# Kernel optimization log

Measured on AMD Instinct MI355X. Metric: run time of the kernel, lower is better.

## Reference

```python
import jax, jax.numpy as jnp
import numpy as np

B, N, H, HEADS, L = 8, 64, 512, 8, 4
VOCAB, NBOND, CLS = 128, 8, 2
SP = H // HEADS
SCALE = float(np.sqrt(H))  # module divides by sqrt(hidden_dim), not sqrt(sp_dim)


def _ln(x):
    # fresh nn.LayerNorm each call -> gamma=1, beta=0
    m = jnp.mean(x, -1, keepdims=True)
    v = jnp.mean((x - m) ** 2, -1, keepdims=True)
    return (x - m) / jnp.sqrt(v + 1e-5)


def _split(x):  # [B,N,H] -> [B,h,N,sp]
    return x.reshape(B, N, HEADS, SP).transpose(0, 2, 1, 3)


def setup_inputs() -> dict:
    key = jax.random.key(0)
    ks = jax.random.split(key, 16)
    s = 0.05
    return {
        "input_batch": jax.random.randint(ks[0], (B, N), 0, VOCAB),
        "adj_m": jax.random.randint(ks[1], (B, N, N), 0, NBOND),
        "atom_emb": jax.random.normal(ks[2], (VOCAB, H), jnp.float32) * s,
        "bond_emb": jax.random.normal(ks[3], (NBOND, H), jnp.float32) * s,
        "Wq": jax.random.normal(ks[4], (L, H, H), jnp.float32) * s,
        "Wk": jax.random.normal(ks[5], (L, H, H), jnp.float32) * s,
        "Wv": jax.random.normal(ks[6], (L, H, H), jnp.float32) * s,
        "Wew": jax.random.normal(ks[7], (L, H, H), jnp.float32) * s,
        "Wstack": jax.random.normal(ks[8], (L, H, H), jnp.float32) * s,
        "Wf1": jax.random.normal(ks[9], (L, H, 4 * H), jnp.float32) * s,
        "Wf2": jax.random.normal(ks[10], (L, 4 * H, H), jnp.float32) * s,
        "Wout": jax.random.normal(ks[11], (H, H), jnp.float32) * s,
        "Wpred": jax.random.normal(ks[12], (H, CLS), jnp.float32) * s,
        "bpred": jnp.zeros((CLS,), jnp.float32),
    }


def _forward(input_batch, adj_m, atom_emb, bond_emb, Wq, Wk, Wv, Wew,
             Wstack, Wf1, Wf2, Wout, Wpred, bpred):
    x = atom_emb[input_batch]        # [B,N,H] atom embeddings
    bond = bond_emb[adj_m]           # [B,N,N,H] bond embeddings
    neg = jnp.where(adj_m > 0, 0.0, -jnp.inf)[:, None, :, :]  # [B,1,N,N]
    for l in range(L):
        xn = _ln(x)
        q = _split(xn @ Wq[l])
        k = _split(xn @ Wk[l])
        v = _split(xn @ Wv[l])
        ew = bond @ Wew[l]           # [B,N,N,H]
        w = ew.reshape(B, N, N, HEADS, SP).transpose(0, 3, 1, 2, 4)  # [B,h,N,N,sp]
        # bond_influence==1: sim_ij = q_i . (k_j + w_ij)
        logits = jnp.einsum('bhid,bhjd->bhij', q, k) \
               + jnp.einsum('bhid,bhijd->bhij', q, w)
        attn = jax.nn.softmax(logits / SCALE + neg, axis=-1)
        o = jnp.einsum('bhij,bhjd->bhid', attn, v)
        o = o.transpose(0, 2, 1, 3).reshape(B, N, H) @ Wstack[l]
        attn_resid = o + xn
        ff = jax.nn.relu(_ln(attn_resid) @ Wf1[l]) @ Wf2[l]
        x = ff + attn_resid          # transformer_output
        # edge attention update: softmax over {w.w, w.x_i, w.x_j}
        ew_s = jnp.sum(ew * ew, -1)                      # [B,N,N]
        a0 = jnp.einsum('bijh,bih->bij', ew, x)
        a1 = jnp.einsum('bijh,bjh->bij', ew, x)
        wgt = jax.nn.softmax(jnp.stack([ew_s, a0, a1], -1) / SCALE, -1)  # [B,N,N,3]
        bond = (wgt[..., 0:1] * ew
                + wgt[..., 1:2] * x[:, :, None, :]
                + wgt[..., 2:3] * x[:, None, :, :])      # new edge state
    cls = jnp.tanh(x[:, 0, :] @ Wout)
    return jax.nn.softmax(cls @ Wpred + bpred, axis=-1)


def reference(input_batch, adj_m, atom_emb, bond_emb, Wq, Wk, Wv, Wew,
              Wstack, Wf1, Wf2, Wout, Wpred, bpred):
    return _forward(input_batch, adj_m, atom_emb, bond_emb, Wq, Wk, Wv, Wew,
                    Wstack, Wf1, Wf2, Wout, Wpred, bpred)
```

## Files before the change

### kernel.cpp

```cpp
#include <hip/hip_runtime.h>
#include <hip/hip_bf16.h>

typedef __hip_bfloat16 bf16;

#define B_     8
#define N_     64
#define H_     512
#define HEADS_ 8
#define SP_    64
#define L_     4
static constexpr float INV_SCALE = 0.044194173824159216f;

typedef __attribute__((ext_vector_type(8))) short short8;
typedef __attribute__((ext_vector_type(4))) float f32x4;

__device__ __forceinline__ void unpack8(uint4 u, float* f) {
    f[0] = __uint_as_float(u.x << 16); f[1] = __uint_as_float(u.x & 0xffff0000u);
    f[2] = __uint_as_float(u.y << 16); f[3] = __uint_as_float(u.y & 0xffff0000u);
    f[4] = __uint_as_float(u.z << 16); f[5] = __uint_as_float(u.z & 0xffff0000u);
    f[6] = __uint_as_float(u.w << 16); f[7] = __uint_as_float(u.w & 0xffff0000u);
}

__device__ __forceinline__ bf16 f2bf(float v) { return __float2bfloat16(v); }

__device__ __forceinline__ uint4 pack8bf(float4 a, float4 b) {
    __align__(16) bf16 t[8];
    t[0] = f2bf(a.x); t[1] = f2bf(a.y); t[2] = f2bf(a.z); t[3] = f2bf(a.w);
    t[4] = f2bf(b.x); t[5] = f2bf(b.y); t[6] = f2bf(b.z); t[7] = f2bf(b.w);
    return *(const uint4*)t;
}

#define RSTR 80

template <int EPI>
__device__ __forceinline__ void gemm64_body(char* lds,
        const bf16* __restrict__ A, const bf16* __restrict__ Bt,
        void* __restrict__ Cv, const float* __restrict__ R,
        int M, int N, int K, int bx, int by, int kbeg, int kend) {
    char* As = lds;
    char* Bs = lds + 2 * 64 * RSTR;
    const int tid = threadIdx.x;
    const int bm = bx * 64, bn = by * 64;
    const int w = tid >> 6, lane = tid & 63;
    const int wr = (w >> 1) * 32, wc = (w & 1) * 32;
    const int m0 = lane & 15, q4 = lane >> 4;

    f32x4 acc[2][2] = {};

    const int rA = tid >> 3;
    const int cA = tid & 7;
    const int ksP = cA >> 2;
    const int cB = (cA & 3) * 16;
    const int cE = cA * 8;

    for (int k0 = kbeg; k0 < kend; k0 += 64) {
        uint4 a0 = *(const uint4*)(A  + (size_t)(bm + rA) * K + k0 + cE);
        uint4 a1 = *(const uint4*)(A  + (size_t)(bm + rA + 32) * K + k0 + cE);
        uint4 b0 = *(const uint4*)(Bt + (size_t)(bn + rA) * K + k0 + cE);
        uint4 b1 = *(const uint4*)(Bt + (size_t)(bn + rA + 32) * K + k0 + cE);
        __syncthreads();
        *(uint4*)(As + ksP * (64 * RSTR) + rA * RSTR + cB) = a0;
        *(uint4*)(As + ksP * (64 * RSTR) + (rA + 32) * RSTR + cB) = a1;
        *(uint4*)(Bs + ksP * (64 * RSTR) + rA * RSTR + cB) = b0;
        *(uint4*)(Bs + ksP * (64 * RSTR) + (rA + 32) * RSTR + cB) = b1;
        __syncthreads();
        short8 af[2][2], bfr[2][2];
        #pragma unroll
        for (int ks = 0; ks < 2; ++ks)
            #pragma unroll
            for (int t = 0; t < 2; ++t) {
                af[ks][t]  = *(const short8*)(As + ks * (64 * RSTR) + (wr + t * 16 + m0) * RSTR + q4 * 16);
                bfr[ks][t] = *(const short8*)(Bs + ks * (64 * RSTR) + (wc + t * 16 + m0) * RSTR + q4 * 16);
            }
        #pragma unroll
        for (int ks = 0; ks < 2; ++ks)
            #pragma unroll
            for (int mt = 0; mt < 2; ++mt)
                #pragma unroll
                for (int nt = 0; nt < 2; ++nt)
                    acc[mt][nt] = __builtin_amdgcn_mfma_f32_16x16x32_bf16(
                        af[ks][mt], bfr[ks][nt], acc[mt][nt], 0, 0, 0);
    }
// ... 4 lines not shown
        for (int mt = 0; mt < 2; ++mt)
            #pragma unroll
            for (int i = 0; i < 4; ++i) {
                int row = bm + wr + mt * 16 + q4 * 4 + i;
                #pragma unroll
                for (int nt = 0; nt < 2; ++nt) {
                    int col = bn + wc + nt * 16 + m0;
                    float v = acc[mt][nt][i];
                    if (EPI == 1) v += R[(size_t)row * N + col];
                    C[(size_t)row * N + col] = v;
                }
            }
    } else {
        bf16* C = (bf16*)Cv;
        #pragma unroll
        for (int mt = 0; mt < 2; ++mt)
            #pragma unroll
            for (int i = 0; i < 4; ++i) {
                int row = bm + wr + mt * 16 + q4 * 4 + i;
                #pragma unroll
                for (int nt = 0; nt < 2; ++nt) {
                    int col = bn + wc + nt * 16 + m0;
                    float v = acc[mt][nt][i];
                    if (EPI == 2) v = fmaxf(v, 0.0f);
                    C[(size_t)row * N + col] = __float2bfloat16(v);
                }
            }
    }
}

template <int EPI, bool SPLIT>
__launch_bounds__(256)
__global__ void mfma_gemm_s(const bf16* __restrict__ A, const bf16* __restrict__ Bt,
                            void* __restrict__ Cv, const float* __restrict__ R,
                            int M, int N, int K) {
    __shared__ __align__(16) char lds[4 * 64 * RSTR];
    int kbeg = 0, kend = K;
    const bf16* B2 = Bt;
    void* C2 = Cv;
    if (SPLIT) {
        int ks = K / gridDim.z;
        kbeg = blockIdx.z * ks;
        kend = kbeg + ks;
        C2 = (void*)((float*)Cv + (size_t)blockIdx.z * M * N);
        gemm64_body<0>(lds, A, B2, C2, nullptr, M, N, K, blockIdx.x, blockIdx.y, kbeg, kend);
    } else {
        B2 = Bt + (size_t)blockIdx.z * N * K;
        if (EPI <= 1) C2 = (void*)((float*)Cv + (size_t)blockIdx.z * M * N);
        gemm64_body<EPI>(lds, A, B2, C2, R, M, N, K, blockIdx.x, blockIdx.y, kbeg, kend);
    }
}


__device__ __forceinline__ void ptable_body(char* lds, const float* __restrict__ q,
        const bf16* __restrict__ Bt, float* __restrict__ P, int b, int h, bool shr) {
    char* As = lds;
    char* Bs = lds + 2 * 64 * RSTR;
    const int tid = threadIdx.x;
    const int w = tid >> 6, lane = tid & 63;
    const int wr = (w >> 1) * 32, wc = (w & 1) * 32;
    const int m0 = lane & 15, q4 = lane >> 4;
    const int rA = tid >> 3;
    const int cA = tid & 7;
    const int ksP = cA >> 2;
    const int cB = (cA & 3) * 16;
    const int cE = cA * 8;

    const float* Aq = q + (size_t)(b * 64) * 512 + h * 64;
    const bf16*  Bb = Bt + (shr ? (size_t)0 : (size_t)b * 64 * 512) + h * 64;

    float4 fa0 = *(const float4*)(Aq + (size_t)rA * 512 + cE);
    float4 fa1 = *(const float4*)(Aq + (size_t)rA * 512 + cE + 4);
    float4 fb0 = *(const float4*)(Aq + (size_t)(rA + 32) * 512 + cE);
    float4 fb1 = *(const float4*)(Aq + (size_t)(rA + 32) * 512 + cE + 4);
    uint4 bv0 = *(const uint4*)(Bb + (size_t)rA * 512 + cE);
    uint4 bv1 = *(const uint4*)(Bb + (size_t)(rA + 32) * 512 + cE);
    uint4 av0 = pack8bf(fa0, fa1);
    uint4 av1 = pack8bf(fb0, fb1);
    *(uint4*)(As + ksP * (64 * RSTR) + rA * RSTR + cB) = av0;
    *(uint4*)(As + ksP * (64 * RSTR) + (rA + 32) * RSTR + cB) = av1;
    *(uint4*)(Bs + ksP * (64 * RSTR) + rA * RSTR + cB) = bv0;
    *(uint4*)(Bs + ksP * (64 * RSTR) + (rA + 32) * RSTR + cB) = bv1;
    __syncthreads();

    f32x4 acc[2][2] = {};
    short8 af[2][2], bfr[2][2];
    #pragma unroll
    for (int ks = 0; ks < 2; ++ks)
        #pragma unroll
        for (int t = 0; t < 2; ++t) {
            af[ks][t]  = *(const short8*)(As + ks * (64 * RSTR) + (wr + t * 16 + m0) * RSTR + q4 * 16);
            bfr[ks][t] = *(const short8*)(Bs + ks * (64 * RSTR) + (wc + t * 16 + m0) * RSTR + q4 * 16);
        }
    #pragma unroll
    for (int ks = 0; ks < 2; ++ks)
        #pragma unroll
        for (int mt = 0; mt < 2; ++mt)
            #pragma unroll
            for (int nt = 0; nt < 2; ++nt)
                acc[mt][nt] = __builtin_amdgcn_mfma_f32_16x16x32_bf16(
                    af[ks][mt], bfr[ks][nt], acc[mt][nt], 0, 0, 0);

    #pragma unroll
    for (int mt = 0; mt < 2; ++mt)
        #pragma unroll
        for (int i = 0; i < 4; ++i) {
            int row = wr + mt * 16 + q4 * 4 + i;
            #pragma unroll
            for (int nt = 0; nt < 2; ++nt) {
                int col = wc + nt * 16 + m0;
                P[(((size_t)b * 8 + h) * 64 + row) * 64 + col] = acc[mt][nt][i];
            }
        }
}

__device__ __forceinline__ void ugemm_body(char* lds, const float* __restrict__ q,
        const bf16* __restrict__ wc3, bf16* __restrict__ ubf, int h, int mb, int nb) {
    char* As = lds;
    char* Bs = lds + 2 * 64 * RSTR;
    const int tid = threadIdx.x;
    const int w = tid >> 6, lane = tid & 63;
    const int wr = (w >> 1) * 32, wc = (w & 1) * 32;
    const int m0 = lane & 15, q4 = lane >> 4;
    const int rA = tid >> 3;
    const int cA = tid & 7;
    const int ksP = cA >> 2;
    const int cB = (cA & 3) * 16;
    const int cE = cA * 8;

    const float* Aq = q + (size_t)(mb * 64) * 512 + h * 64;
    const bf16*  Bt = wc3 + (size_t)(nb * 64) * 512 + h * 64;

    float4 fa0 = *(const float4*)(Aq + (size_t)rA * 512 + cE);
    float4 fa1 = *(const float4*)(Aq + (size_t)rA * 512 + cE + 4);
    float4 fb0 = *(const float4*)(Aq + (size_t)(rA + 32) * 512 + cE);
    float4 fb1 = *(const float4*)(Aq + (size_t)(rA + 32) * 512 + cE + 4);
    uint4 b0 = *(const uint4*)(Bt + (size_t)rA * 512 + cE);
    uint4 b1 = *(const uint4*)(Bt + (size_t)(rA + 32) * 512 + cE);
    uint4 a0 = pack8bf(fa0, fa1);
    uint4 a1 = pack8bf(fb0, fb1);
    *(uint4*)(As + ksP * (64 * RSTR) + rA * RSTR + cB) = a0;
    *(uint4*)(As + ksP * (64 * RSTR) + (rA + 32) * RSTR + cB) = a1;
    *(uint4*)(Bs + ksP * (64 * RSTR) + rA * RSTR + cB) = b0;
    *(uint4*)(Bs + ksP * (64 * RSTR) + (rA + 32) * RSTR + cB) = b1;
    __syncthreads();

    f32x4 acc[2][2] = {};
    short8 af[2][2], bfr[2][2];
    #pragma unroll
    for (int ks = 0; ks < 2; ++ks)
        #pragma unroll
        for (int t = 0; t < 2; ++t) {
            af[ks][t]  = *(const short8*)(As + ks * (64 * RSTR) + (wr + t * 16 + m0) * RSTR + q4 * 16);
            bfr[ks][t] = *(const short8*)(Bs + ks * (64 * RSTR) + (wc + t * 16 + m0) * RSTR + q4 * 16);
        }
    #pragma unroll
    for (int ks = 0; ks < 2; ++ks)
        #pragma unroll
        for (int mt = 0; mt < 2; ++mt)
            #pragma unroll
            for (int nt = 0; nt < 2; ++nt)
                acc[mt][nt] = __builtin_amdgcn_mfma_f32_16x16x32_bf16(
                    af[ks][mt], bfr[ks][nt], acc[mt][nt], 0, 0, 0);

    #pragma unroll
    for (int mt = 0; mt < 2; ++mt)
        #pragma unroll
        for (int i = 0; i < 4; ++i) {
            int row = mb * 64 + wr + mt * 16 + q4 * 4 + i;
            #pragma unroll
            for (int nt = 0; nt < 2; ++nt) {
                int col = nb * 64 + wc + nt * 16 + m0;
                ubf[(size_t)row * 4096 + h * 512 + col] = f2bf(acc[mt][nt][i]);
            }
        }
}

__device__ __forceinline__ void coeff0_body(const int* __restrict__ adj,
        const float* __restrict__ gbuf, int row, int j,
        float* __restrict__ w0o, float* __restrict__ w1o, float* __restrict__ w2o) {
    int b = row >> 6, i = row & 63;
    int p = row * 64 + j;
    int t = adj[p];
    const float* G0  = gbuf + 5 * 32768 + (size_t)b * 4096;
    const float* TEE = gbuf + 6 * 32768;
    float s0 = TEE[t * 64 + t];
    float s1 = G0[t * 64 + i];
    float s2 = G0[t * 64 + j];
    float t0 = s0 * INV_SCALE, t1 = s1 * INV_SCALE, t2 = s2 * INV_SCALE;
    float m = fmaxf(t0, fmaxf(t1, t2));
    float e0 = expf(t0 - m), e1 = expf(t1 - m), e2 = expf(t2 - m);
    float inv = 1.0f / (e0 + e1 + e2);
    w0o[p] = e0 * inv;
    w1o[p] = e1 * inv;
    w2o[p] = e2 * inv;
}

__device__ __forceinline__ void coeff1_body(const int* __restrict__ adj,
        const float* __restrict__ c0a, const float* __restrict__ c1a, const float* __restrict__ c2a,
        const float* __restrict__ gbuf, int row, int j,
        float* __restrict__ w0o, float* __restrict__ w1o, float* __restrict__ w2o) {
    int b = row >> 6, i = row & 63;
    int p = row * 64 + j;
    int t = adj[p];
    const float* TXX = gbuf + 0 * 32768 + (size_t)b * 4096;
    const float* TEX = gbuf + 1 * 32768 + (size_t)b * 4096;
    const float* TXx = gbuf + 2 * 32768 + (size_t)b * 4096;
    const float* TEx = gbuf + 3 * 32768 + (size_t)b * 4096;
    const float* TEE = gbuf + 4 * 32768 + (size_t)b * 4096;
    float c0 = c0a[p], c1 = c1a[p], c2 = c2a[p];
    float s1 = c0 * TEx[t * 64 + i] + c1 * TXx[i * 64 + i] + c2 * TXx[j * 64 + i];
    float s2 = c0 * TEx[t * 64 + j] + c1 * TXx[i * 64 + j] + c2 * TXx[j * 64 + j];
    float s0 = c0 * c0 * TEE[t * 64 + t] + c1 * c1 * TXX[i * 64 + i] + c2 * c2 * TXX[j * 64 + j]
             + 2.f * c0 * c1 * TEX[t * 64 + i] + 2.f * c0 * c2 * TEX[t * 64 + j]
             + 2.f * c1 * c2 * TXX[i * 64 + j];
    float t0 = s0 * INV_SCALE, t1 = s1 * INV_SCALE, t2 = s2 * INV_SCALE;
    float m = fmaxf(t0, fmaxf(t1, t2));
    float e0 = expf(t0 - m), e1 = expf(t1 - m), e2 = expf(t2 - m);
    float inv = 1.0f / (e0 + e1 + e2);
    w0o[p] = e0 * inv;
    w1o[p] = e1 * inv;
    w2o[p] = e2 * inv;
}

__device__ __forceinline__ void coeff2_body(const int* __restrict__ adj,
        const float* __restrict__ c0a, const float* __restrict__ c1a, const float* __restrict__ c2a,
        const float* __restrict__ c0b, const float* __restrict__ c1b, const float* __restrict__ c2b,
        const float* __restrict__ gbuf, int row, int j,
        float* __restrict__ w0o, float* __restrict__ w1o, float* __restrict__ w2o) {
    int b = row >> 6, i = row & 63;
    int p = row * 64 + j;
    int t = adj[p];
    const float* TXX = gbuf + 0 * 32768 + (size_t)b * 4096;
    const float* TXY = gbuf + 1 * 32768 + (size_t)b * 4096;
    const float* TYY = gbuf + 2 * 32768 + (size_t)b * 4096;
    const float* TEX = gbuf + 3 * 32768 + (size_t)b * 4096;
    const float* TEY = gbuf + 4 * 32768 + (size_t)b * 4096;
    const float* TEE = gbuf + 5 * 32768 + (size_t)b * 4096;
    const float* TXx = gbuf + 6 * 32768 + (size_t)b * 4096;
    const float* TYx = gbuf + 7 * 32768 + (size_t)b * 4096;
    const float* TEx = gbuf + 8 * 32768 + (size_t)b * 4096;
    float a0 = c0b[p];
    float AE = a0 * c0a[p], Aa = a0 * c1a[p], Ab = a0 * c2a[p];
    float Ac = c1b[p], Ad = c2b[p];
    float s1 = AE * TEx[t * 64 + i] + Aa * TXx[i * 64 + i] + Ab * TXx[j * 64 + i]
             + Ac * TYx[i * 64 + i] + Ad * TYx[j * 64 + i];
    float s2 = AE * TEx[t * 64 + j] + Aa * TXx[i * 64 + j] + Ab * TXx[j * 64 + j]
             + Ac * TYx[i * 64 + j] + Ad * TYx[j * 64 + j];
    float s0 = AE * AE * TEE[t * 64 + t] + Aa * Aa * TXX[i * 64 + i] + Ab * Ab * TXX[j * 64 + j]
             + Ac * Ac * TYY[i * 64 + i] + Ad * Ad * TYY[j * 64 + j]
             + 2.f * AE * Aa * TEX[t * 64 + i] + 2.f * AE * Ab * TEX[t * 64 + j]
             + 2.f * AE * Ac * TEY[t * 64 + i] + 2.f * AE * Ad * TEY[t * 64 + j]
             + 2.f * Aa * Ab * TXX[i * 64 + j]
             + 2.f * Aa * Ac * TXY[i * 64 + i] + 2.f * Aa * Ad * TXY[i * 64 + j]
             + 2.f * Ab * Ac * TXY[j * 64 + i] + 2.f * Ab * Ad * TXY[j * 64 + j]
             + 2.f * Ac * Ad * TYY[i * 64 + j];
    float t0 = s0 * INV_SCALE, t1 = s1 * INV_SCALE, t2 = s2 * INV_SCALE;
    float m = fmaxf(t0, fmaxf(t1, t2));
    float e0 = expf(t0 - m), e1 = expf(t1 - m), e2 = expf(t2 - m);
    float inv = 1.0f / (e0 + e1 + e2);
    w0o[p] = e0 * inv;
    w1o[p] = e1 * inv;
    w2o[p] = e2 * inv;
}

__launch_bounds__(256)
__global__ void setup_kernel(const int* __restrict__ ids, const float* __restrict__ atom_emb,
                             const float* __restrict__ bond_emb,
                             const float* __restrict__ Wq, const float* __restrict__ Wk,
                             const float* __restrict__ Wv, const float* __restrict__ Wew,
                             const float* __restrict__ Wst,
                             const float* __restrict__ Wf1, const float* __restrict__ Wf2,
                             float* __restrict__ xn, bf16* __restrict__ xn_bf,
                             bf16* __restrict__ qkvt, bf16* __restrict__ ewt,
                             bf16* __restrict__ stackt,
// ... 97 lines not shown
    }
}

__launch_bounds__(256)
__global__ void qkv0_e0(const bf16* __restrict__ xn_bf, const bf16* __restrict__ qkvt,
                        float* __restrict__ qkv,
                        const bf16* __restrict__ bond_bf, const bf16* __restrict__ ewt0,
                        bf16* __restrict__ E0) {
    __shared__ __align__(16) char lds[4 * 64 * RSTR];
    int bid = blockIdx.x;
    if (bid < 192) {
        int z = bid >> 6, rem = bid & 63;
        int mb = rem >> 3, by = rem & 7;
        gemm64_body<0>(lds, xn_bf, qkvt + (size_t)z * 262144,
                       qkv + (size_t)z * 262144, nullptr, 512, 512, 512, mb, by, 0, 512);
    } else {
        gemm64_body<3>(lds, bond_bf, ewt0, E0, nullptr, 64, 512, 512,
                       0, bid - 192, 0, 512);
    }
}

__launch_bounds__(256)
__global__ void basis1_qkv_g0(const bf16* __restrict__ x_bf, const bf16* __restrict__ E0,
                              const bf16* __restrict__ ewt1,
                              bf16* __restrict__ xw1, bf16* __restrict__ e0w1,
                              const bf16* __restrict__ xn_bf, const bf16* __restrict__ qkvt_l,
                              float* __restrict__ qkv, float* __restrict__ gbuf) {
    __shared__ __align__(16) char lds[4 * 64 * RSTR];
    int bid = blockIdx.x;
    if (bid < 264) {
        int bx = bid >> 3, by = bid & 7;
        if (bx < 8)
            gemm64_body<3>(lds, x_bf, ewt1, xw1, nullptr, 512, 512, 512, bx, by, 0, 512);
        else if (bx == 8)
            gemm64_body<3>(lds, E0, ewt1, e0w1, nullptr, 64, 512, 512, 0, by, 0, 512);
        else {
            int tq = bx - 9;
            int z = tq >> 3, mb = tq & 7;
            gemm64_body<0>(lds, xn_bf, qkvt_l + (size_t)z * 262144,
                           qkv + (size_t)z * 262144, nullptr, 512, 512, 512, mb, by, 0, 512);
        }
    } else if (bid < 272) {
        int b = bid - 264;
        gemm64_body<0>(lds, E0, x_bf + (size_t)b * 32768,
                       gbuf + 5 * 32768 + (size_t)b * 4096, nullptr,
                       64, 64, 512, 0, 0, 0, 512);
    } else {
        gemm64_body<0>(lds, E0, E0, gbuf + 6 * 32768, nullptr,
                       64, 64, 512, 0, 0, 0, 512);
    }
}

__launch_bounds__(256)
__global__ void ptable1c(const float* __restrict__ q,
                         const bf16* __restrict__ B0, const bf16* __restrict__ B1,
                         float* __restrict__ P0, float* __restrict__ P1,
                         const int* __restrict__ adj, const float* __restrict__ gbuf,
                         float* __restrict__ w0o, float* __restrict__ w1o,
                         float* __restrict__ w2o) {
    __shared__ __align__(16) char lds[4 * 64 * RSTR];
    int bid = blockIdx.x;
    if (bid < 128) {
        int z = bid >> 6, rem = bid & 63;
        int b = rem >> 3, h = rem & 7;
        const bf16* Bt = (z == 0) ? B0 : B1;
        float* P = (z == 0) ? P0 : P1;
        ptable_body(lds, q, Bt, P, b, h, z == 1);
    } else {
        int k = bid - 128;
        int tid = threadIdx.x;
        int j = tid & 63;
        #pragma unroll
        for (int pass = 0; pass < 2; ++pass) {
            int row = k * 8 + pass * 4 + (tid >> 6);
            coeff0_body(adj, gbuf, row, j, w0o, w1o, w2o);
        }
    }
}

__launch_bounds__(256)
__global__ void basis2_qkv_g1(const bf16* __restrict__ xw1, const bf16* __restrict__ x_bf,
                              const bf16* __restrict__ e0w1, const bf16* __restrict__ ewt2,
                              bf16* __restrict__ xw12, bf16* __restrict__ x2w2,
                              bf16* __restrict__ e0w12,
                              const bf16* __restrict__ xn_bf, const bf16* __restrict__ qkvt_l,
                              float* __restrict__ qkv, float* __restrict__ gbuf) {
    __shared__ __align__(16) char lds[4 * 64 * RSTR];
    int bid = blockIdx.x;
    if (bid < 328) {
        int bx = bid >> 3, by = bid & 7;
        if (bx < 8)
            gemm64_body<3>(lds, xw1, ewt2, xw12, nullptr, 512, 512, 512, bx, by, 0, 512);
        else if (bx < 16)
            gemm64_body<3>(lds, x_bf, ewt2, x2w2, nullptr, 512, 512, 512, bx - 8, by, 0, 512);
        else if (bx == 16)
            gemm64_body<3>(lds, e0w1, ewt2, e0w12, nullptr, 64, 512, 512, 0, by, 0, 512);
        else {
            int tq = bx - 17;
            int z = tq >> 3, mb = tq & 7;
            gemm64_body<0>(lds, xn_bf, qkvt_l + (size_t)z * 262144,
                           qkv + (size_t)z * 262144, nullptr, 512, 512, 512, mb, by, 0, 512);
        }
    } else {
        int k = bid - 328;
        int b = k & 7, z = k >> 3;
        size_t ob = (size_t)b * 32768;
        const bf16 *A, *Bt;
        switch (z) {
            case 0: A = xw1 + ob; Bt = xw1 + ob; break;
            case 1: A = e0w1;     Bt = xw1 + ob; break;
            case 2: A = xw1 + ob; Bt = x_bf + ob; break;
            case 3: A = e0w1;     Bt = x_bf + ob; break;
            default: A = e0w1;    Bt = e0w1;     break;
        }
        float* C = gbuf + (size_t)z * 32768 + (size_t)b * 4096;
        gemm64_body<0>(lds, A, Bt, C, nullptr, 64, 64, 512, 0, 0, 0, 512);
    }
}

__launch_bounds__(256)
__global__ void ptable2c(const float* __restrict__ q,
                         const bf16* __restrict__ B0, const bf16* __restrict__ B1,
                         const bf16* __restrict__ B2,
                         float* __restrict__ P0, float* __restrict__ P1,
                         float* __restrict__ P2,
                         const int* __restrict__ adj,
                         const float* __restrict__ c0a, const float* __restrict__ c1a,
                         const float* __restrict__ c2a, const float* __restrict__ gbuf,
                         float* __restrict__ w0o, float* __restrict__ w1o,
                         float* __restrict__ w2o) {
    __shared__ __align__(16) char lds[4 * 64 * RSTR];
    int bid = blockIdx.x;
    if (bid < 192) {
        int z = bid >> 6, rem = bid & 63;
        int b = rem >> 3, h = rem & 7;
        const bf16* Bt = (z == 0) ? B0 : (z == 1 ? B1 : B2);
        float* P = (z == 0) ? P0 : (z == 1 ? P1 : P2);
        ptable_body(lds, q, Bt, P, b, h, z == 2);
    } else {
        int k = bid - 192;
        int tid = threadIdx.x;
        int j = tid & 63;
        #pragma unroll
        for (int pass = 0; pass < 2; ++pass) {
            int row = k * 8 + pass * 4 + (tid >> 6);
            coeff1_body(adj, c0a, c1a, c2a, gbuf, row, j, w0o, w1o, w2o);
        }
    }
}

__launch_bounds__(256)
__global__ void l3qkv_g2(const bf16* __restrict__ xn_bf, const bf16* __restrict__ qkvt_l,
                         float* __restrict__ qkv,
                         const bf16* __restrict__ xw12, const bf16* __restrict__ x2w2,
                         const bf16* __restrict__ e0w12, const bf16* __restrict__ x_bf,
                         float* __restrict__ gbuf) {
    __shared__ __align__(16) char lds[4 * 64 * RSTR];
    int bid = blockIdx.x;
    if (bid < 192) {
        int z = bid >> 6, rem = bid & 63;
        int mb = rem >> 3, by = rem & 7;
        gemm64_body<0>(lds, xn_bf, qkvt_l + (size_t)z * 262144,
                       qkv + (size_t)z * 262144, nullptr, 512, 512, 512, mb, by, 0, 512);
    } else {
        int k = bid - 192;
        int b = k & 7, z = k >> 3;
        size_t ob = (size_t)b * 32768;
        const bf16 *A, *Bt;
        switch (z) {
            case 0: A = xw12 + ob; Bt = xw12 + ob; break;
            case 1: A = xw12 + ob; Bt = x2w2 + ob; break;
            case 2: A = x2w2 + ob; Bt = x2w2 + ob; break;
            case 3: A = e0w12;     Bt = xw12 + ob; break;
            case 4: A = e0w12;     Bt = x2w2 + ob; break;
            case 5: A = e0w12;     Bt = e0w12;     break;
            case 6: A = xw12 + ob; Bt = x_bf + ob; break;
            case 7: A = x2w2 + ob; Bt = x_bf + ob; break;
            default: A = e0w12;    Bt = x_bf + ob; break;
        }
        float* C = gbuf + (size_t)z * 32768 + (size_t)b * 4096;
        gemm64_body<0>(lds, A, Bt, C, nullptr, 64, 64, 512, 0, 0, 0, 512);
    }
}

__launch_bounds__(256)
__global__ void u_c2(const float* __restrict__ q, const bf16* __restrict__ wc3,
                     bf16* __restrict__ ubf,
                     const int* __restrict__ adj,
                     const float* __restrict__ c0a, const float* __restrict__ c1a,
                     const float* __restrict__ c2a,
                     const float* __restrict__ c0b, const float* __restrict__ c1b,
                     const float* __restrict__ c2b,
                     const float* __restrict__ gbuf,
                     float* __restrict__ w0o, float* __restrict__ w1o,
                     float* __restrict__ w2o) {
    __shared__ __align__(16) char lds[4 * 64 * RSTR];
    int bid = blockIdx.x;
    if (bid < 512) {
        int h = bid >> 6, mb = (bid >> 3) & 7, nb = bid & 7;
        ugemm_body(lds, q, wc3, ubf, h, mb, nb);
    } else {
        int k = bid - 512;
        int tid = threadIdx.x;
        int j = tid & 63;
// ... 107 lines not shown
    int bi = blockIdx.x;
    int b  = bi >> 6;
    int ty = threadIdx.y;
    int h  = blockIdx.y * 4 + ty;
    int lane = threadIdx.x;
    __shared__ float qs[4][64], as[4][64];
    qs[ty][lane] = q[(size_t)bi * H_ + h * 64 + lane];
    __syncthreads();

    int j = lane;
    int pair = bi * 64 + j;
    int aj = adj[pair];
    const float4* k4 = (const float4*)(k + (size_t)(b * 64 + j) * H_ + h * 64);
    const uint4*  w4 = (const uint4*)((GATHER ? ew + (size_t)aj * H_
                                              : ew + (size_t)pair * H_) + h * 64);
    float acc = 0.f;
    #pragma unroll
    for (int t = 0; t < 8; ++t) {
        uint4 wu = w4[t];
        float4 ka = k4[2 * t], kb = k4[2 * t + 1];
        float wf[8];
        unpack8(wu, wf);
        const float* qq = &qs[ty][t * 8];
        acc += qq[0] * (ka.x + wf[0]) + qq[1] * (ka.y + wf[1])
             + qq[2] * (ka.z + wf[2]) + qq[3] * (ka.w + wf[3])
             + qq[4] * (kb.x + wf[4]) + qq[5] * (kb.y + wf[5])
             + qq[6] * (kb.z + wf[6]) + qq[7] * (kb.w + wf[7]);
    }
    float logit = acc * INV_SCALE;
    if (aj <= 0) logit = -INFINITY;

    float m = logit;
    #pragma unroll
    for (int off = 32; off; off >>= 1) m = fmaxf(m, __shfl_xor(m, off));
    float p = expf(logit - m);
    float s = p;
    #pragma unroll
    for (int off = 32; off; off >>= 1) s += __shfl_xor(s, off);
    as[ty][lane] = p / s;
    __syncthreads();

    const float* vbase = v + (size_t)(b * 64) * H_ + h * 64;
    float oacc = 0.f;
    int d = lane;
    #pragma unroll 8
    for (int jj = 0; jj < 64; ++jj)
        oacc += as[ty][jj] * vbase[(size_t)jj * H_ + d];
    o[(size_t)bi * H_ + h * 64 + d] = __float2bfloat16(oacc);
}

template <int MODE>
__global__ void attn13_kernel(const float* __restrict__ qkv, const int* __restrict__ adj,
        const float* __restrict__ c0a, const float* __restrict__ c1a, const float* __restrict__ c2a,
        const float* __restrict__ c0b, const float* __restrict__ c1b, const float* __restrict__ c2b,
        const float* __restrict__ PX, const float* __restrict__ PY, const float* __restrict__ PE,
        bf16* __restrict__ o) {
    const float* q = qkv;
    const float* k = qkv + (size_t)512 * H_;
    const float* v = qkv + (size_t)1024 * H_;
    int bi = blockIdx.x;
    int b  = bi >> 6, i = bi & 63;
    int ty = threadIdx.y;
    int h  = blockIdx.y * 4 + ty;
    int lane = threadIdx.x;
    __shared__ float qs[4][64], as[4][64];
    qs[ty][lane] = q[(size_t)bi * H_ + h * 64 + lane];
    __syncthreads();

    int j = lane;
    int p = bi * 64 + j;
    int t = adj[p];
    size_t pb = (((size_t)b * 8 + h) * 64 + i) * 64;
    float acc;
    if (MODE == 1) {
        acc = c0a[p] * PE[pb + t] + c1a[p] * PX[pb + i] + c2a[p] * PX[pb + j];
    } else {
        float a0 = c0b[p];
        float AE = a0 * c0a[p], Aa = a0 * c1a[p], Ab = a0 * c2a[p];
        float Ac = c1b[p], Ad = c2b[p];
        acc = AE * PE[pb + t] + Aa * PX[pb + i] + Ab * PX[pb + j]
            + Ac * PY[pb + i] + Ad * PY[pb + j];
    }
    const float4* k4 = (const float4*)(k + (size_t)(b * 64 + j) * H_ + h * 64);
    #pragma unroll
    for (int tt = 0; tt < 8; ++tt) {
        float4 ka = k4[2 * tt], kb = k4[2 * tt + 1];
        const float* qq = &qs[ty][tt * 8];
        acc += qq[0] * ka.x + qq[1] * ka.y + qq[2] * ka.z + qq[3] * ka.w
             + qq[4] * kb.x + qq[5] * kb.y + qq[6] * kb.z + qq[7] * kb.w;
    }
    float logit = acc * INV_SCALE;
    if (t <= 0) logit = -INFINITY;

    float m = logit;
    #pragma unroll
    for (int off = 32; off; off >>= 1) m = fmaxf(m, __shfl_xor(m, off));
    float pe = expf(logit - m);
    float s = pe;
    #pragma unroll
    for (int off = 32; off; off >>= 1) s += __shfl_xor(s, off);
    as[ty][lane] = pe / s;
    __syncthreads();

    const float* vbase = v + (size_t)(b * 64) * H_ + h * 64;
    float oacc = 0.f;
    int d = lane;
    #pragma unroll 8
    for (int jj = 0; jj < 64; ++jj)
        oacc += as[ty][jj] * vbase[(size_t)jj * H_ + d];
    o[(size_t)bi * H_ + h * 64 + d] = __float2bfloat16(oacc);
}

__global__ void attn3s2_kernel(const float* __restrict__ qkv, const int* __restrict__ adj,
        const float* __restrict__ c0a, const float* __restrict__ c1a, const float* __restrict__ c2a,
        const float* __restrict__ c0b, const float* __restrict__ c1b, const float* __restrict__ c2b,
        const float* __restrict__ v0c, const float* __restrict__ v1c, const float* __restrict__ v2c,
        const float* __restrict__ MX, const float* __restrict__ MY,
        const float* __restrict__ MZ, const float* __restrict__ DE,
        bf16* __restrict__ o) {
    const float* q = qkv;
    const float* k = qkv + (size_t)512 * H_;
    const float* v = qkv + (size_t)1024 * H_;
    int bi = blockIdx.x;
    int b  = bi >> 6, i = bi & 63;
    int ty = threadIdx.y;
    int h  = blockIdx.y * 4 + ty;
    int lane = threadIdx.x;
    __shared__ float qs[4][64], as[4][64];
    qs[ty][lane] = q[(size_t)bi * H_ + h * 64 + lane];
    __syncthreads();

    int j = lane;
    int p = bi * 64 + j;
    int t = adj[p];
    float v0 = v0c[p];
    float q0 = v0 * c0b[p];
    float AE = q0 * c0a[p], Aa = q0 * c1a[p], Ab = q0 * c2a[p];
    float Ac = v0 * c1b[p], Ad = v0 * c2b[p];
    float Ae = v1c[p], Af = v2c[p];
    size_t rb = ((size_t)b * 512 + i * 8 + h) * 64;
    float acc = AE * DE[rb + t]
              + Aa * MX[rb + i] + Ac * MY[rb + i] + Ae * MZ[rb + i]
// ... 85 lines not shown
        float m = fmaxf(s0, s1);
        float e0 = expf(s0 - m), e1 = expf(s1 - m);
        float inv = 1.0f / (e0 + e1);
        out[b * 2 + 0] = e0 * inv;
        out[b * 2 + 1] = e1 * inv;
    }
}

extern "C" void kernel_launch(void* const* d_in, const int* in_sizes, int n_in,
                              void* d_out, int out_size, void* d_ws, size_t ws_size,
                              hipStream_t stream) {
    const int*   ids      = (const int*)d_in[0];
    const int*   adj      = (const int*)d_in[1];
    const float* atom_emb = (const float*)d_in[2];
    const float* bond_emb = (const float*)d_in[3];
    const float* Wq     = (const float*)d_in[4];
    const float* Wk     = (const float*)d_in[5];
    const float* Wv     = (const float*)d_in[6];
    const float* Wew    = (const float*)d_in[7];
    const float* Wstack = (const float*)d_in[8];
    const float* Wf1    = (const float*)d_in[9];
    const float* Wf2    = (const float*)d_in[10];
    const float* Wout   = (const float*)d_in[11];
    const float* Wpred  = (const float*)d_in[12];
    const float* bpred  = (const float*)d_in[13];

    char* ws = (char*)d_ws;
    size_t off = 0;
    auto alloc = [&](size_t bytes) {
        size_t o = off;
        off += (bytes + 255) & ~(size_t)255;
        return o;
    };
    const size_t ROWS  = (size_t)B_ * N_;
    const size_t PAIRS = (size_t)B_ * N_ * N_;
    const size_t KN    = (size_t)H_ * H_;

    float* x       = (float*)(ws + alloc(ROWS * H_ * 4));
    float* xn      = (float*)(ws + alloc(ROWS * H_ * 4));
    bf16*  xn_bf   = (bf16*) (ws + alloc(ROWS * H_ * 2));
    bf16*  x_bf    = (bf16*) (ws + alloc(ROWS * H_ * 2));
    float* qkv     = (float*)(ws + alloc(3 * ROWS * H_ * 4));
    bf16*  o_bf    = (bf16*) (ws + alloc(ROWS * H_ * 2));
    float* resid   = (float*)(ws + alloc(ROWS * H_ * 4));
    bf16*  ffin_bf = (bf16*) (ws + alloc(ROWS * H_ * 2));
    bf16*  ffh_bf  = (bf16*) (ws + alloc(ROWS * 4 * H_ * 2));
    float* part    = (float*)(ws + alloc(4 * ROWS * H_ * 4));
    float* clspart = (float*)(ws + alloc(4 * 8 * H_ * 4));
    bf16*  ubf     = (bf16*) (ws + alloc(ROWS * 8 * 512 * 2));
    float* MX      = (float*)(ws + alloc((size_t)4096 * 64 * 4));
    float* MY      = (float*)(ws + alloc((size_t)4096 * 64 * 4));
    float* MZ      = (float*)(ws + alloc((size_t)4096 * 64 * 4));
    float* DE      = (float*)(ws + alloc((size_t)4096 * 64 * 4));
    float* PT0     = (float*)(ws + alloc((size_t)4096 * 64 * 4));
    float* PT1     = (float*)(ws + alloc((size_t)4096 * 64 * 4));
    float* PT2     = (float*)(ws + alloc((size_t)4096 * 64 * 4));
    float* gbuf    = (float*)(ws + alloc((size_t)9 * 8 * 4096 * 4));
    bf16*  wc3     = (bf16*) (ws + alloc(KN * 2));
    bf16*  bond_bf = (bf16*) (ws + alloc(64 * H_ * 2));
    bf16*  E0      = (bf16*) (ws + alloc(64 * H_ * 2));
    bf16*  e0w1    = (bf16*) (ws + alloc(64 * H_ * 2));
    bf16*  e0w12   = (bf16*) (ws + alloc(64 * H_ * 2));
    bf16*  xw1     = (bf16*) (ws + alloc(KN * 2));
    bf16*  xw12    = (bf16*) (ws + alloc(KN * 2));
    bf16*  x2w2    = (bf16*) (ws + alloc(KN * 2));
    float* cw      = (float*)(ws + alloc(9 * PAIRS * 4));
    bf16*  qkvt    = (bf16*) (ws + alloc((size_t)L_ * 3 * KN * 2));
    bf16*  ewt     = (bf16*) (ws + alloc((size_t)L_ * KN * 2));
    bf16*  stackt  = (bf16*) (ws + alloc((size_t)L_ * KN * 2));
    bf16*  f1t     = (bf16*) (ws + alloc((size_t)L_ * 4 * KN * 2));
    bf16*  f2t     = (bf16*) (ws + alloc((size_t)L_ * 4 * KN * 2));
    (void)ws_size;

    float* cw0a = cw;
    float* cw1a = cw + PAIRS;
    float* cw2a = cw + 2 * PAIRS;
    float* cw0b = cw + 3 * PAIRS;
    float* cw1b = cw + 4 * PAIRS;
    float* cw2b = cw + 5 * PAIRS;
    float* cw0c = cw + 6 * PAIRS;
    float* cw1c = cw + 7 * PAIRS;
    float* cw2c = cw + 8 * PAIRS;

    setup_kernel<<<2432, 256, 0, stream>>>(ids, atom_emb, bond_emb,
                                           Wq, Wk, Wv, Wew, Wstack, Wf1, Wf2,
                                           xn, xn_bf, qkvt, ewt, stackt, f1t, f2t,
                                           bond_bf, wc3);

    for (int l = 0; l < L_; ++l) {
        if (l == 0) {
            qkv0_e0<<<200, 256, 0, stream>>>(xn_bf, qkvt, qkv, bond_bf, ewt, E0);
            attn_kernel<true><<<dim3(512, 2), dim3(64, 4), 0, stream>>>(qkv, E0, adj, o_bf);
        } else if (l == 1) {
            basis1_qkv_g0<<<273, 256, 0, stream>>>(
                x_bf, E0, ewt + KN, xw1, e0w1, xn_bf, qkvt + (size_t)3 * KN, qkv, gbuf);
            ptable1c<<<192, 256, 0, stream>>>(qkv, xw1, e0w1, PT0, PT1,
                                              adj, gbuf, cw0a, cw1a, cw2a);
            attn13_kernel<1><<<dim3(512, 2), dim3(64, 4), 0, stream>>>(
                qkv, adj, cw0a, cw1a, cw2a, nullptr, nullptr, nullptr,
                PT0, nullptr, PT1, o_bf);
        } else if (l == 2) {
            basis2_qkv_g1<<<368, 256, 0, stream>>>(
                xw1, x_bf, e0w1, ewt + 2 * KN, xw12, x2w2, e0w12,
                xn_bf, qkvt + (size_t)6 * KN, qkv, gbuf);
            ptable2c<<<256, 256, 0, stream>>>(
                qkv, xw12, x2w2, e0w12, PT0, PT1, PT2,
                adj, cw0a, cw1a, cw2a, gbuf, cw0b, cw1b, cw2b);
            attn13_kernel<2><<<dim3(512, 2), dim3(64, 4), 0, stream>>>(
                qkv, adj, cw0a, cw1a, cw2a, cw0b, cw1b, cw2b,
                PT0, PT1, PT2, o_bf);
        } else {
            l3qkv_g2<<<264, 256, 0, stream>>>(
                xn_bf, qkvt + (size_t)9 * KN, qkv, xw12, x2w2, e0w12, x_bf, gbuf);
            u_c2<<<576, 256, 0, stream>>>(
                qkv, wc3, ubf, adj, cw0a, cw1a, cw2a, cw0b, cw1b, cw2b,
                gbuf, cw0c, cw1c, cw2c);
            mbuf_gemm<<<dim3(8, 8, 4), 256, 0, stream>>>(ubf, xw12, x2w2, x_bf, e0w12,
                                                         MX, MY, MZ, DE);
            attn3s2_kernel<<<dim3(512, 2), dim3(64, 4), 0, stream>>>(
                qkv, adj, cw0a, cw1a, cw2a, cw0b, cw1b, cw2b, cw0c, cw1c, cw2c,
                MX, MY, MZ, DE, o_bf);
        }

        mfma_gemm_s<0, true><<<dim3(8, 8, 4), 256, 0, stream>>>(
            o_bf, stackt + (size_t)l * KN, part, nullptr, 512, 512, 512);
        reduce_stack_ln<<<512, 256, 0, stream>>>(part, xn, resid, ffin_bf);
        mfma_gemm_s<2, false><<<dim3(8, 32), 256, 0, stream>>>(
            ffin_bf, f1t + (size_t)l * 4 * KN, ffh_bf, nullptr, 512, 2048, 512);
        mfma_gemm_s<0, true><<<dim3(8, 8, 4), 256, 0, stream>>>(
            ffh_bf, f2t + (size_t)l * 4 * KN, part, nullptr, 512, 512, 2048);
        if (l < L_ - 1)
            reduce_ln_kernel<true><<<512, 256, 0, stream>>>(part, resid, x, x_bf, xn, xn_bf);
        else
            reduce_ln_kernel<false><<<512, 256, 0, stream>>>(part, resid, x, x_bf, xn, xn_bf);
    }

    cls_part_kernel<<<dim3(8, 8, 4), 256, 0, stream>>>(x, Wout, clspart);
    cls_pred2_kernel<<<8, 256, 0, stream>>>(clspart, Wpred, bpred, (float*)d_out);
}
```

Measured before the change: 338.3 us.

## Fuse projection tables and edge coefficients into attention kernels for layers 1-2

Removes the separate ptable1c/ptable2c launches. The attention kernel now computes the edge softmax coefficients itself and writes them out from one block slice. It also computes the per-head q·basis dot products with scalar bf16 dot loops and shares the i-index terms across lanes with shuffles. This saves two kernel launches and the round trip of the P tables through global memory, at the cost of replacing MFMA table GEMMs with scalar dot products done per (i,j) lane, some of them redundantly.

```diff
diff --git a/kernel.cpp b/kernel.cpp
--- a/kernel.cpp
+++ b/kernel.cpp
@@ -28,6 +28,21 @@
     t[0] = f2bf(a.x); t[1] = f2bf(a.y); t[2] = f2bf(a.z); t[3] = f2bf(a.w);
     t[4] = f2bf(b.x); t[5] = f2bf(b.y); t[6] = f2bf(b.z); t[7] = f2bf(b.w);
     return *(const uint4*)t;
+}
+
+__device__ __forceinline__ float dot64(const float* __restrict__ qq,
+                                       const bf16* __restrict__ row) {
+    float acc = 0.f;
+    #pragma unroll
+    for (int t = 0; t < 8; ++t) {
+        uint4 u = ((const uint4*)row)[t];
+        float f[8];
+        unpack8(u, f);
+        const float* q8 = &qq[t * 8];
+        acc += q8[0]*f[0] + q8[1]*f[1] + q8[2]*f[2] + q8[3]*f[3]
+             + q8[4]*f[4] + q8[5]*f[5] + q8[6]*f[6] + q8[7]*f[7];
+    }
+    return acc;
 }
 
 #define RSTR 80
@@ -138,68 +153,6 @@
 }
 
 
-__device__ __forceinline__ void ptable_body(char* lds, const float* __restrict__ q,
-        const bf16* __restrict__ Bt, float* __restrict__ P, int b, int h, bool shr) {
-    char* As = lds;
-    char* Bs = lds + 2 * 64 * RSTR;
-    const int tid = threadIdx.x;
-    const int w = tid >> 6, lane = tid & 63;
-    const int wr = (w >> 1) * 32, wc = (w & 1) * 32;
-    const int m0 = lane & 15, q4 = lane >> 4;
-    const int rA = tid >> 3;
-    const int cA = tid & 7;
-    const int ksP = cA >> 2;
-    const int cB = (cA & 3) * 16;
-    const int cE = cA * 8;
-
-    const float* Aq = q + (size_t)(b * 64) * 512 + h * 64;
-    const bf16*  Bb = Bt + (shr ? (size_t)0 : (size_t)b * 64 * 512) + h * 64;
-
-    float4 fa0 = *(const float4*)(Aq + (size_t)rA * 512 + cE);
-    float4 fa1 = *(const float4*)(Aq + (size_t)rA * 512 + cE + 4);
-    float4 fb0 = *(const float4*)(Aq + (size_t)(rA + 32) * 512 + cE);
-    float4 fb1 = *(const float4*)(Aq + (size_t)(rA + 32) * 512 + cE + 4);
-    uint4 bv0 = *(const uint4*)(Bb + (size_t)rA * 512 + cE);
-    uint4 bv1 = *(const uint4*)(Bb + (size_t)(rA + 32) * 512 + cE);
-    uint4 av0 = pack8bf(fa0, fa1);
-    uint4 av1 = pack8bf(fb0, fb1);
-    *(uint4*)(As + ksP * (64 * RSTR) + rA * RSTR + cB) = av0;
-    *(uint4*)(As + ksP * (64 * RSTR) + (rA + 32) * RSTR + cB) = av1;
-    *(uint4*)(Bs + ksP * (64 * RSTR) + rA * RSTR + cB) = bv0;
-    *(uint4*)(Bs + ksP * (64 * RSTR) + (rA + 32) * RSTR + cB) = bv1;
-    __syncthreads();
-
-    f32x4 acc[2][2] = {};
-    short8 af[2][2], bfr[2][2];
-    #pragma unroll
-    for (int ks = 0; ks < 2; ++ks)
-        #pragma unroll
-        for (int t = 0; t < 2; ++t) {
-            af[ks][t]  = *(const short8*)(As + ks * (64 * RSTR) + (wr + t * 16 + m0) * RSTR + q4 * 16);
-            bfr[ks][t] = *(const short8*)(Bs + ks * (64 * RSTR) + (wc + t * 16 + m0) * RSTR + q4 * 16);
-        }
-    #pragma unroll
-    for (int ks = 0; ks < 2; ++ks)
-        #pragma unroll
-        for (int mt = 0; mt < 2; ++mt)
-            #pragma unroll
-            for (int nt = 0; nt < 2; ++nt)
-                acc[mt][nt] = __builtin_amdgcn_mfma_f32_16x16x32_bf16(
-                    af[ks][mt], bfr[ks][nt], acc[mt][nt], 0, 0, 0);
-
-    #pragma unroll
-    for (int mt = 0; mt < 2; ++mt)
-        #pragma unroll
-        for (int i = 0; i < 4; ++i) {
-            int row = wr + mt * 16 + q4 * 4 + i;
-            #pragma unroll
-            for (int nt = 0; nt < 2; ++nt) {
-                int col = wc + nt * 16 + m0;
-                P[(((size_t)b * 8 + h) * 64 + row) * 64 + col] = acc[mt][nt][i];
-            }
-        }
-}
-
 __device__ __forceinline__ void ugemm_body(char* lds, const float* __restrict__ q,
         const bf16* __restrict__ wc3, bf16* __restrict__ ubf, int h, int mb, int nb) {
     char* As = lds;
@@ -262,12 +215,8 @@
         }
 }
 
-__device__ __forceinline__ void coeff0_body(const int* __restrict__ adj,
-        const float* __restrict__ gbuf, int row, int j,
-        float* __restrict__ w0o, float* __restrict__ w1o, float* __restrict__ w2o) {
-    int b = row >> 6, i = row & 63;
-    int p = row * 64 + j;
-    int t = adj[p];
+__device__ __forceinline__ void coeff0_vals(const float* __restrict__ gbuf,
+        int b, int i, int j, int t, float* c) {
     const float* G0  = gbuf + 5 * 32768 + (size_t)b * 4096;
     const float* TEE = gbuf + 6 * 32768;
     float s0 = TEE[t * 64 + t];
@@ -277,24 +226,16 @@
     float m = fmaxf(t0, fmaxf(t1, t2));
     float e0 = expf(t0 - m), e1 = expf(t1 - m), e2 = expf(t2 - m);
     float inv = 1.0f / (e0 + e1 + e2);
-    w0o[p] = e0 * inv;
-    w1o[p] = e1 * inv;
-    w2o[p] = e2 * inv;
-}
-
-__device__ __forceinline__ void coeff1_body(const int* __restrict__ adj,
-        const float* __restrict__ c0a, const float* __restrict__ c1a, const float* __restrict__ c2a,
-        const float* __restrict__ gbuf, int row, int j,
-        float* __restrict__ w0o, float* __restrict__ w1o, float* __restrict__ w2o) {
-    int b = row >> 6, i = row & 63;
-    int p = row * 64 + j;
-    int t = adj[p];
+    c[0] = e0 * inv; c[1] = e1 * inv; c[2] = e2 * inv;
+}
+
+__device__ __forceinline__ void coeff1_vals(const float* __restrict__ gbuf,
+        float c0, float c1, float c2, int b, int i, int j, int t, float* c) {
     const float* TXX = gbuf + 0 * 32768 + (size_t)b * 4096;
     const float* TEX = gbuf + 1 * 32768 + (size_t)b * 4096;
     const float* TXx = gbuf + 2 * 32768 + (size_t)b * 4096;
     const float* TEx = gbuf + 3 * 32768 + (size_t)b * 4096;
     const float* TEE = gbuf + 4 * 32768 + (size_t)b * 4096;
-    float c0 = c0a[p], c1 = c1a[p], c2 = c2a[p];
     float s1 = c0 * TEx[t * 64 + i] + c1 * TXx[i * 64 + i] + c2 * TXx[j * 64 + i];
     float s2 = c0 * TEx[t * 64 + j] + c1 * TXx[i * 64 + j] + c2 * TXx[j * 64 + j];
     float s0 = c0 * c0 * TEE[t * 64 + t] + c1 * c1 * TXX[i * 64 + i] + c2 * c2 * TXX[j * 64 + j]
@@ -304,9 +245,7 @@
     float m = fmaxf(t0, fmaxf(t1, t2));
     float e0 = expf(t0 - m), e1 = expf(t1 - m), e2 = expf(t2 - m);
     float inv = 1.0f / (e0 + e1 + e2);
-    w0o[p] = e0 * inv;
-    w1o[p] = e1 * inv;
-    w2o[p] = e2 * inv;
+    c[0] = e0 * inv; c[1] = e1 * inv; c[2] = e2 * inv;
 }
 
 __device__ __forceinline__ void coeff2_body(const int* __restrict__ adj,
@@ -510,33 +449,6 @@
 }
 
 __launch_bounds__(256)
-__global__ void ptable1c(const float* __restrict__ q,
-                         const bf16* __restrict__ B0, const bf16* __restrict__ B1,
-                         float* __restrict__ P0, float* __restrict__ P1,
-                         const int* __restrict__ adj, const float* __restrict__ gbuf,
-                         float* __restrict__ w0o, float* __restrict__ w1o,
-                         float* __restrict__ w2o) {
-    __shared__ __align__(16) char lds[4 * 64 * RSTR];
-    int bid = blockIdx.x;
-    if (bid < 128) {
-        int z = bid >> 6, rem = bid & 63;
-        int b = rem >> 3, h = rem & 7;
-        const bf16* Bt = (z == 0) ? B0 : B1;
-        float* P = (z == 0) ? P0 : P1;
-        ptable_body(lds, q, Bt, P, b, h, z == 1);
-    } else {
-        int k = bid - 128;
-        int tid = threadIdx.x;
-        int j = tid & 63;
-        #pragma unroll
-        for (int pass = 0; pass < 2; ++pass) {
-            int row = k * 8 + pass * 4 + (tid >> 6);
-            coeff0_body(adj, gbuf, row, j, w0o, w1o, w2o);
-        }
-    }
-}
-
-__launch_bounds__(256)
 __global__ void basis2_qkv_g1(const bf16* __restrict__ xw1, const bf16* __restrict__ x_bf,
                               const bf16* __restrict__ e0w1, const bf16* __restrict__ ewt2,
                               bf16* __restrict__ xw12, bf16* __restrict__ x2w2,
@@ -577,37 +489,6 @@
 }
 
 __launch_bounds__(256)
-__global__ void ptable2c(const float* __restrict__ q,
-                         const bf16* __restrict__ B0, const bf16* __restrict__ B1,
-                         const bf16* __restrict__ B2,
-                         float* __restrict__ P0, float* __restrict__ P1,
-                         float* __restrict__ P2,
-                         const int* __restrict__ adj,
-                         const float* __restrict__ c0a, const float* __restrict__ c1a,
-                         const float* __restrict__ c2a, const float* __restrict__ gbuf,
-                         float* __restrict__ w0o, float* __restrict__ w1o,
-                         float* __restrict__ w2o) {
-    __shared__ __align__(16) char lds[4 * 64 * RSTR];
-    int bid = blockIdx.x;
-    if (bid < 192) {
-        int z = bid >> 6, rem = bid & 63;
-        int b = rem >> 3, h = rem & 7;
-        const bf16* Bt = (z == 0) ? B0 : (z == 1 ? B1 : B2);
-        float* P = (z == 0) ? P0 : (z == 1 ? P1 : P2);
-        ptable_body(lds, q, Bt, P, b, h, z == 2);
-    } else {
-        int k = bid - 192;
-        int tid = threadIdx.x;
-        int j = tid & 63;
-        #pragma unroll
-        for (int pass = 0; pass < 2; ++pass) {
-            int row = k * 8 + pass * 4 + (tid >> 6);
-            coeff1_body(adj, c0a, c1a, c2a, gbuf, row, j, w0o, w1o, w2o);
-        }
-    }
-}
-
-__launch_bounds__(256)
 __global__ void l3qkv_g2(const bf16* __restrict__ xn_bf, const bf16* __restrict__ qkvt_l,
                          float* __restrict__ qkv,
                          const bf16* __restrict__ xw12, const bf16* __restrict__ x2w2,
@@ -821,8 +702,9 @@
 template <int MODE>
 __global__ void attn13_kernel(const float* __restrict__ qkv, const int* __restrict__ adj,
         const float* __restrict__ c0a, const float* __restrict__ c1a, const float* __restrict__ c2a,
-        const float* __restrict__ c0b, const float* __restrict__ c1b, const float* __restrict__ c2b,
-        const float* __restrict__ PX, const float* __restrict__ PY, const float* __restrict__ PE,
+        const bf16* __restrict__ BE, const bf16* __restrict__ BX, const bf16* __restrict__ BY,
+        const float* __restrict__ gbuf,
+        float* __restrict__ w0o, float* __restrict__ w1o, float* __restrict__ w2o,
         bf16* __restrict__ o) {
     const float* q = qkv;
     const float* k = qkv + (size_t)512 * H_;
@@ -839,24 +721,40 @@
     int j = lane;
     int p = bi * 64 + j;
     int t = adj[p];
-    size_t pb = (((size_t)b * 8 + h) * 64 + i) * 64;
+
+    float cc[3];
+    if (MODE == 1) {
+        coeff0_vals(gbuf, b, i, j, t, cc);
+    } else {
+        coeff1_vals(gbuf, c0a[p], c1a[p], c2a[p], b, i, j, t, cc);
+    }
+    if (blockIdx.y == 0 && ty == 0) {
+        w0o[p] = cc[0]; w1o[p] = cc[1]; w2o[p] = cc[2];
+    }
+
+    const float* qq = qs[ty];
+    float pE  = dot64(qq, BE + (size_t)t * H_ + h * 64);
+    float pXj = dot64(qq, BX + ((size_t)(b * 64 + j)) * H_ + h * 64);
+    float pXi = __shfl(pXj, i);
+
     float acc;
     if (MODE == 1) {
-        acc = c0a[p] * PE[pb + t] + c1a[p] * PX[pb + i] + c2a[p] * PX[pb + j];
+        acc = cc[0] * pE + cc[1] * pXi + cc[2] * pXj;
     } else {
-        float a0 = c0b[p];
+        float pYj = dot64(qq, BY + ((size_t)(b * 64 + j)) * H_ + h * 64);
+        float pYi = __shfl(pYj, i);
+        float a0 = cc[0];
         float AE = a0 * c0a[p], Aa = a0 * c1a[p], Ab = a0 * c2a[p];
-        float Ac = c1b[p], Ad = c2b[p];
-        acc = AE * PE[pb + t] + Aa * PX[pb + i] + Ab * PX[pb + j]
-            + Ac * PY[pb + i] + Ad * PY[pb + j];
-    }
+        acc = AE * pE + Aa * pXi + Ab * pXj + cc[1] * pYi + cc[2] * pYj;
+    }
+
     const float4* k4 = (const float4*)(k + (size_t)(b * 64 + j) * H_ + h * 64);
     #pragma unroll
     for (int tt = 0; tt < 8; ++tt) {
         float4 ka = k4[2 * tt], kb = k4[2 * tt + 1];
-        const float* qq = &qs[ty][tt * 8];
-        acc += qq[0] * ka.x + qq[1] * ka.y + qq[2] * ka.z + qq[3] * ka.w
-             + qq[4] * kb.x + qq[5] * kb.y + qq[6] * kb.z + qq[7] * kb.w;
+        const float* q8 = &qs[ty][tt * 8];
+        acc += q8[0] * ka.x + q8[1] * ka.y + q8[2] * ka.z + q8[3] * ka.w
+             + q8[4] * kb.x + q8[5] * kb.y + q8[6] * kb.z + q8[7] * kb.w;
     }
     float logit = acc * INV_SCALE;
     if (t <= 0) logit = -INFINITY;
@@ -1048,9 +946,6 @@
     float* MY      = (float*)(ws + alloc((size_t)4096 * 64 * 4));
     float* MZ      = (float*)(ws + alloc((size_t)4096 * 64 * 4));
     float* DE      = (float*)(ws + alloc((size_t)4096 * 64 * 4));
-    float* PT0     = (float*)(ws + alloc((size_t)4096 * 64 * 4));
-    float* PT1     = (float*)(ws + alloc((size_t)4096 * 64 * 4));
-    float* PT2     = (float*)(ws + alloc((size_t)4096 * 64 * 4));
     float* gbuf    = (float*)(ws + alloc((size_t)9 * 8 * 4096 * 4));
     bf16*  wc3     = (bf16*) (ws + alloc(KN * 2));
     bf16*  bond_bf = (bf16*) (ws + alloc(64 * H_ * 2));
@@ -1090,21 +985,16 @@
         } else if (l == 1) {
             basis1_qkv_g0<<<273, 256, 0, stream>>>(
                 x_bf, E0, ewt + KN, xw1, e0w1, xn_bf, qkvt + (size_t)3 * KN, qkv, gbuf);
-            ptable1c<<<192, 256, 0, stream>>>(qkv, xw1, e0w1, PT0, PT1,
-                                              adj, gbuf, cw0a, cw1a, cw2a);
             attn13_kernel<1><<<dim3(512, 2), dim3(64, 4), 0, stream>>>(
-                qkv, adj, cw0a, cw1a, cw2a, nullptr, nullptr, nullptr,
-                PT0, nullptr, PT1, o_bf);
+                qkv, adj, nullptr, nullptr, nullptr,
+                e0w1, xw1, nullptr, gbuf, cw0a, cw1a, cw2a, o_bf);
         } else if (l == 2) {
             basis2_qkv_g1<<<368, 256, 0, stream>>>(
                 xw1, x_bf, e0w1, ewt + 2 * KN, xw12, x2w2, e0w12,
                 xn_bf, qkvt + (size_t)6 * KN, qkv, gbuf);
-            ptable2c<<<256, 256, 0, stream>>>(
-                qkv, xw12, x2w2, e0w12, PT0, PT1, PT2,
-                adj, cw0a, cw1a, cw2a, gbuf, cw0b, cw1b, cw2b);
             attn13_kernel<2><<<dim3(512, 2), dim3(64, 4), 0, stream>>>(
-                qkv, adj, cw0a, cw1a, cw2a, cw0b, cw1b, cw2b,
-                PT0, PT1, PT2, o_bf);
+                qkv, adj, cw0a, cw1a, cw2a,
+                e0w12, xw12, x2w2, gbuf, cw0b, cw1b, cw2b, o_bf);
         } else {
             l3qkv_g2<<<264, 256, 0, stream>>>(
                 xn_bf, qkvt + (size_t)9 * KN, qkv, xw12, x2w2, e0w12, x_bf, gbuf);
```

New measurement: 351.9 us. 4.0% more time.
